# Performance work log

Measured on AMD Instinct MI355X. Metric: run time of the kernel, lower is better.

## Reference

```python
import jax, jax.numpy as jnp
import numpy as np

D = 128
NG = 100_000   # gene nodes
ND = 20_000    # disease nodes
EGG = 1_000_000  # gene->gene edges
EGD = 500_000    # gene->disease edges
NEG_SLOPE = 0.2  # PyG GATv2Conv default


def setup_inputs() -> dict:
    key = jax.random.key(0)
    ks = jax.random.split(key, 16)
    f = lambda k, shape, s=1.0: jax.random.normal(k, shape, dtype=jnp.float32) * s
    return {
        "x_gene": f(ks[0], (NG, D)),
        "x_dis": f(ks[1], (ND, D)),
        "src_gg": jax.random.randint(ks[2], (EGG,), 0, NG, dtype=jnp.int32),
        "dst_gg": jax.random.randint(ks[3], (EGG,), 0, NG, dtype=jnp.int32),
        "src_gd": jax.random.randint(ks[4], (EGD,), 0, NG, dtype=jnp.int32),
        "dst_gd": jax.random.randint(ks[5], (EGD,), 0, ND, dtype=jnp.int32),
        # stacked over the 2 layers: [layer, ...]
        "Wsrc_gg": f(ks[6], (2, D, D), 0.1),
        "Wdst_gg": f(ks[7], (2, D, D), 0.1),
        "att_gg": f(ks[8], (2, D), 0.1),
        "b_gg": f(ks[9], (2, D), 0.1),
        "Wsrc_gd": f(ks[10], (2, D, D), 0.1),
        "Wdst_gd": f(ks[11], (2, D, D), 0.1),
        "att_gd": f(ks[12], (2, D), 0.1),
        "b_gd": f(ks[13], (2, D), 0.1),
    }


def _gatv2(x_src, x_dst, src, dst, Wsrc, Wdst, att, b, n_dst):
    """PyG GATv2Conv, heads=1, add_self_loops=False."""
    xl = x_src @ Wsrc            # [Ns, D] source transform (lin_l)
    xr = x_dst @ Wdst            # [Nd, D] target transform (lin_r)
    e = jax.nn.leaky_relu(xl[src] + xr[dst], NEG_SLOPE)   # [E, D]
    score = e @ att                                        # [E]
    # segment softmax over incoming edges of each destination node
    m = jax.ops.segment_max(score, dst, num_segments=n_dst)
    a = jnp.exp(score - m[dst])
    s = jax.ops.segment_sum(a, dst, num_segments=n_dst)
    alpha = a / s[dst]                                     # [E]
    out = jax.ops.segment_sum(alpha[:, None] * xl[src], dst, num_segments=n_dst)
    return out + b


def reference(x_gene, x_dis, src_gg, dst_gg, src_gd, dst_gd,
              Wsrc_gg, Wdst_gg, att_gg, b_gg,
              Wsrc_gd, Wdst_gd, att_gd, b_gd):
    xg, xd = x_gene, x_dis
    for l in range(2):  # num_gat_layers=2, structurally distinct weights
        ng = _gatv2(xg, xg, src_gg, dst_gg, Wsrc_gg[l], Wdst_gg[l],
                    att_gg[l], b_gg[l], xg.shape[0])
        nd = _gatv2(xg, xd, src_gd, dst_gd, Wsrc_gd[l], Wdst_gd[l],
                    att_gd[l], b_gd[l], xd.shape[0])
        xg, xd = ng, nd  # HeteroConv: each node type receives from one edge type; aggr='sum' trivially
    # concatenate node-type outputs so the result is a single array
    return jnp.concatenate([xg, xd], axis=0)
```

## Files before the change

### kernel.cpp

```cpp
#include <hip/hip_runtime.h>

#define NGn 100000
#define NDn 20000
#define EGGn 1000000
#define EGDn 500000
#define Dn 128
#define NT (NGn + NDn)
#define ET (EGGn + EGDn)
#define NBK ((NT + 255) / 256)
#define P2B 128
#define CHUNK ((ET + P2B - 1) / P2B)

typedef unsigned short u16;
typedef unsigned int u32;
typedef __attribute__((ext_vector_type(8))) short short8;
typedef __attribute__((ext_vector_type(4))) float f32x4;

__device__ __forceinline__ float blo(u32 u) { return __uint_as_float(u << 16); }
__device__ __forceinline__ float bhi(u32 u) { return __uint_as_float(u & 0xffff0000u); }
__device__ __forceinline__ u16 f2bf(float f) {
    u32 u = __float_as_uint(f);
    u32 r = (u + 0x7fffu + ((u >> 16) & 1u)) >> 16;
    return (u16)r;
}

__device__ __forceinline__ int probe_bf16(const u16* __restrict__ x) {
    int lane = threadIdx.x & 63;
    u16 v = x[2 * lane];
    int e = (v >> 7) & 0xFF;
    unsigned long long m = __ballot(e >= 110 && e <= 135);
    return __popcll(m) >= 32;
}

#define NBX 15000
#define NBW 12
__global__ __launch_bounds__(256) void prep_all(
    const void* __restrict__ xg0, const void* __restrict__ xd0,
    const void* w0, const void* w1, const void* w2, const void* w3,
    const void* a0, const void* a1, const void* a2, const void* a3,
    u16* __restrict__ og, u16* __restrict__ od,
    u16* __restrict__ wbT, u16* __restrict__ vb,
    const int* __restrict__ dst_gg, const int* __restrict__ dst_gd,
    u32* __restrict__ bucketCnt)
{
    __shared__ u32 hist[NBK];
    int bx = blockIdx.x;
    int t = threadIdx.x;
    if (bx < NBX) {
        int f = probe_bf16((const u16*)xg0);
        if (f) return;
        int i4 = (bx * 256 + t) * 4;
        const int n1 = NGn * Dn;
        const float4* src; u16* dst; int j4;
        if (i4 < n1) { src = (const float4*)xg0; dst = og; j4 = i4; }
        else         { src = (const float4*)xd0; dst = od; j4 = i4 - n1; }
        float4 v = src[j4 >> 2];
        uint2 pack;
        pack.x = (u32)f2bf(v.x) | ((u32)f2bf(v.y) << 16);
        pack.y = (u32)f2bf(v.z) | ((u32)f2bf(v.w) << 16);
        *reinterpret_cast<uint2*>(dst + j4) = pack;
    } else if (bx < NBX + NBW) {
        int f = probe_bf16((const u16*)xg0);
        int sub = bx - NBX;
        if (sub < 8) {
            const void* srcs[4] = {w0, w1, w2, w3};
            const void* sp = srcs[sub >> 1];
            int ebase = (sub & 1) * (Dn * Dn);
            size_t mbase = (size_t)sub * (Dn * Dn);
            for (int i = t; i < Dn * Dn; i += 256) {
                u16 v = f ? ((const u16*)sp)[ebase + i] : f2bf(((const float*)sp)[ebase + i]);
                wbT[mbase + (size_t)((i & 127) << 7) + (i >> 7)] = v;
            }
        } else {
            const void* srcs[4] = {a0, a1, a2, a3};
            const void* sp = srcs[sub - 8];
            u16 v = f ? ((const u16*)sp)[t] : f2bf(((const float*)sp)[t]);
            vb[(sub - 8) * 256 + t] = v;
        }
    } else {
        int sub = bx - NBX - NBW;
        for (int i = t; i < NBK; i += 256) hist[i] = 0;
        __syncthreads();
        int lo = sub * CHUNK, hi = min(ET, lo + CHUNK);
        for (int i = lo + t; i < hi; i += 256) {
            int d = (i < EGGn) ? dst_gg[i] : (NGn + dst_gd[i - EGGn]);
            atomicAdd(&hist[d >> 8], 1u);
        }
        __syncthreads();
        for (int i = t; i < NBK; i += 256)
            if (hist[i]) atomicAdd(&bucketCnt[i], hist[i]);
    }
}

__global__ __launch_bounds__(256) void scan_buckets(
    const u32* __restrict__ bucketCnt, u32* __restrict__ bbase, u32* __restrict__ bcur)
{
    __shared__ u32 sh[256];
    int t = threadIdx.x;
    u32 carry = 0;
    for (int base = 0; base < NBK; base += 256) {
        int i = base + t;
        u32 v = (i < NBK) ? bucketCnt[i] : 0;
        sh[t] = v;
        __syncthreads();
#pragma unroll
        for (int off = 1; off < 256; off <<= 1) {
            u32 a = (t >= off) ? sh[t - off] : 0;
            __syncthreads();
            sh[t] += a;
            __syncthreads();
        }
        if (i < NBK) { u32 e = carry + sh[t] - v; bbase[i] = e; bcur[i] = e; }
        u32 chunk = sh[255];
        __syncthreads();
        carry += chunk;
    }
    if (t == 0) bbase[NBK] = carry;
}

#define GG_BLK ((NGn + 63) / 64)
#define GD_BLK ((NDn + 63) / 64)
#define LDB(KS) do { \
    b0 = Wof[0*256 + (KS)*4]; b1 = Wof[1*256 + (KS)*4]; \
    b2 = Wof[2*256 + (KS)*4]; b3 = Wof[3*256 + (KS)*4]; \
    b4 = Wof[4*256 + (KS)*4]; b5 = Wof[5*256 + (KS)*4]; \
    b6 = Wof[6*256 + (KS)*4]; b7 = Wof[7*256 + (KS)*4]; } while (0)
#define MFMA8(A) do { \
    c0 = __builtin_amdgcn_mfma_f32_16x16x32_bf16(A, b0, c0, 0, 0, 0); \
    c1 = __builtin_amdgcn_mfma_f32_16x16x32_bf16(A, b1, c1, 0, 0, 0); \
    c2 = __builtin_amdgcn_mfma_f32_16x16x32_bf16(A, b2, c2, 0, 0, 0); \
    c3 = __builtin_amdgcn_mfma_f32_16x16x32_bf16(A, b3, c3, 0, 0, 0); \
    c4 = __builtin_amdgcn_mfma_f32_16x16x32_bf16(A, b4, c4, 0, 0, 0); \
    c5 = __builtin_amdgcn_mfma_f32_16x16x32_bf16(A, b5, c5, 0, 0, 0); \
    c6 = __builtin_amdgcn_mfma_f32_16x16x32_bf16(A, b6, c6, 0, 0, 0); \
    c7 = __builtin_amdgcn_mfma_f32_16x16x32_bf16(A, b7, c7, 0, 0, 0); } while (0)
#define STORE_NT(NT, CV) do { \
    int cidx = (NT)*16 + r; \
    int rw0 = row0 + g*4; \
    if (rw0 + 0 < M) Y[(size_t)(rw0 + 0) * Dn + cidx] = f2bf(CV[0]); \
    if (rw0 + 1 < M) Y[(size_t)(rw0 + 1) * Dn + cidx] = f2bf(CV[1]); \
    if (rw0 + 2 < M) Y[(size_t)(rw0 + 2) * Dn + cidx] = f2bf(CV[2]); \
    if (rw0 + 3 < M) Y[(size_t)(rw0 + 3) * Dn + cidx] = f2bf(CV[3]); } while (0)

__device__ __forceinline__ void gemm_body(
    int gbx,
    const u16* __restrict__ Xg, const u16* __restrict__ Xd,
    const u16* __restrict__ WTg0, const u16* __restrict__ WTg1, const u16* __restrict__ WTg2,
    const u16* __restrict__ WTd,
    u16* __restrict__ Y0, u16* __restrict__ Y1, u16* __restrict__ Y2, u16* __restrict__ Y3)
{
    int wv = threadIdx.x >> 6, lane = threadIdx.x & 63;
    int r = lane & 15, g = lane >> 4;
    bool gene = gbx < GG_BLK;
    int blk = gene ? gbx : gbx - GG_BLK;
    int M = gene ? NGn : NDn;
    const u16* X = gene ? Xg : Xd;
    int row0 = blk * 64 + wv * 16;
    if (row0 >= M) return;
    int arow = row0 + r; if (arow >= M) arow = M - 1;
    const short8* Xa = reinterpret_cast<const short8*>(X + (size_t)arow * Dn);
    short8 a0 = Xa[g], a1 = Xa[4 + g], a2 = Xa[8 + g], a3 = Xa[12 + g];

    int no = gene ? 3 : 1;
    for (int o = 0; o < no; ++o) {
        const u16* Wt = gene ? ((o == 0) ? WTg0 : (o == 1) ? WTg1 : WTg2) : WTd;
        u16* Y = gene ? ((o == 0) ? Y0 : (o == 1) ? Y1 : Y2) : Y3;
        const short8* Wof = reinterpret_cast<const short8*>(Wt) + (size_t)r * 16 + g;
        f32x4 c0 = {0,0,0,0}, c1 = {0,0,0,0}, c2 = {0,0,0,0}, c3 = {0,0,0,0};
        f32x4 c4 = {0,0,0,0}, c5 = {0,0,0,0}, c6 = {0,0,0,0}, c7 = {0,0,0,0};
        short8 b0, b1, b2, b3, b4, b5, b6, b7;
        LDB(0); MFMA8(a0);
        LDB(1); MFMA8(a1);
        LDB(2); MFMA8(a2);
        LDB(3); MFMA8(a3);
        STORE_NT(0, c0); STORE_NT(1, c1); STORE_NT(2, c2); STORE_NT(3, c3);
        STORE_NT(4, c4); STORE_NT(5, c5); STORE_NT(6, c6); STORE_NT(7, c7);
    }
}

__global__ __launch_bounds__(256) void scatter_gemm(
    const int* __restrict__ src_gg, const int* __restrict__ dst_gg,
    const int* __restrict__ src_gd, const int* __restrict__ dst_gd,
    u32* __restrict__ bcur, u32* __restrict__ staging,
    const u16* __restrict__ xg0, const u16* __restrict__ xd0,
    const u16* __restrict__ Xgc, const u16* __restrict__ Xdc,
    const u16* __restrict__ WTg0, const u16* __restrict__ WTg1, const u16* __restrict__ WTg2,
    const u16* __restrict__ WTd,
    u16* __restrict__ Y0, u16* __restrict__ Y1, u16* __restrict__ Y2, u16* __restrict__ Y3)
{
    __shared__ u32 hist[NBK];
    __shared__ u32 lbase[NBK];
    int bx = blockIdx.x;
    if (bx < P2B) {
        int t = threadIdx.x;
        for (int i = t; i < NBK; i += 256) hist[i] = 0;
        __syncthreads();
        int lo = bx * CHUNK, hi = min(ET, lo + CHUNK);
        for (int i = lo + t; i < hi; i += 256) {
            int d = (i < EGGn) ? dst_gg[i] : (NGn + dst_gd[i - EGGn]);
            atomicAdd(&hist[d >> 8], 1u);
        }
        __syncthreads();
        for (int i = t; i < NBK; i += 256)
            lbase[i] = hist[i] ? atomicAdd(&bcur[i], hist[i]) : 0;
        __syncthreads();
        for (int i = t; i < NBK; i += 256) hist[i] = 0;
        __syncthreads();
        for (int i = lo + t; i < hi; i += 256) {
            int s, d;
            if (i < EGGn) { s = src_gg[i]; d = dst_gg[i]; }
            else          { s = src_gd[i - EGGn]; d = NGn + dst_gd[i - EGGn]; }
            int bk = d >> 8;
            u32 off = atomicAdd(&hist[bk], 1u);
            staging[lbase[bk] + off] = ((u32)s << 8) | (u32)(d & 255);
        }
    } else {
        int f = probe_bf16(xg0);
        const u16* Xg = f ? xg0 : Xgc;
        const u16* Xd = f ? xd0 : Xdc;
        gemm_body(bx - P2B, Xg, Xd, WTg0, WTg1, WTg2, WTd, Y0, Y1, Y2, Y3);
    }
}

__global__ __launch_bounds__(256) void fine_csr(
    const u32* __restrict__ bbase, const u32* __restrict__ staging,
    u32* __restrict__ rp, u32* __restrict__ deg, int* __restrict__ col)
{
    __shared__ u32 hist[256];
    __shared__ u32 sh[256];
    __shared__ u32 ex[256];
    int b = blockIdx.x, t = threadIdx.x;
    int base = (int)bbase[b], end = (int)bbase[b + 1];
    hist[t] = 0;
    __syncthreads();
    for (int i = base + t; i < end; i += 256)
        atomicAdd(&hist[staging[i] & 255u], 1u);
    __syncthreads();
    u32 v = hist[t];
    sh[t] = v;
    __syncthreads();
#pragma unroll
    for (int off = 1; off < 256; off <<= 1) {
        u32 a = (t >= off) ? sh[t - off] : 0;
        __syncthreads();
        sh[t] += a;
        __syncthreads();
    }
    ex[t] = sh[t] - v;
    int node = b * 256 + t;
    if (node < NT) { deg[node] = v; rp[node] = base + ex[t]; }
    hist[t] = 0;
    __syncthreads();
    for (int i = base + t; i < end; i += 256) {
        u32 pv = staging[i];
        u32 n = pv & 255u;
        u32 off2 = atomicAdd(&hist[n], 1u);
        col[base + ex[n] + off2] = (int)(pv >> 8);
    }
}

__global__ __launch_bounds__(256) void gemm_only(
    const u16* __restrict__ Xg, const u16* __restrict__ Xd,
    const u16* __restrict__ WTg0, const u16* __restrict__ WTg1, const u16* __restrict__ WTg2,
    const u16* __restrict__ WTd,
    u16* __restrict__ Y0, u16* __restrict__ Y1, u16* __restrict__ Y2, u16* __restrict__ Y3)
{
    gemm_body(blockIdx.x, Xg, Xd, WTg0, WTg1, WTg2, WTd, Y0, Y1, Y2, Y3);
}

#define SCORE8(RV, VALID, SC) do {                                                   \
    float x0_=blo(RV.x), x1_=bhi(RV.x), x2_=blo(RV.y), x3_=bhi(RV.y);                \
    float x4_=blo(RV.z), x5_=bhi(RV.z), x6_=blo(RV.w), x7_=bhi(RV.w);                \
    float t0_ = x0_ + xr0; t0_ = fmaxf(t0_, 0.2f * t0_);                             \
    float t1_ = x1_ + xr1; t1_ = fmaxf(t1_, 0.2f * t1_);                             \
    float t2_ = x2_ + xr2; t2_ = fmaxf(t2_, 0.2f * t2_);                             \
    float t3_ = x3_ + xr3; t3_ = fmaxf(t3_, 0.2f * t3_);                             \
    float t4_ = x4_ + xr4; t4_ = fmaxf(t4_, 0.2f * t4_);                             \
    float t5_ = x5_ + xr5; t5_ = fmaxf(t5_, 0.2f * t5_);                             \
    float t6_ = x6_ + xr6; t6_ = fmaxf(t6_, 0.2f * t6_);                             \
    float t7_ = x7_ + xr7; t7_ = fmaxf(t7_, 0.2f * t7_);                             \
    float sc_ = t0_*at0 + t1_*at1 + t2_*at2 + t3_*at3                                \
              + t4_*at4 + t5_*at5 + t6_*at6 + t7_*at7;                               \
    sc_ += __shfl_xor(sc_, 4);                                                       \
    sc_ += __shfl_xor(sc_, 8);                                                       \
    sc_ += __shfl_xor(sc_, 16);                                                      \
    sc_ += __shfl_xor(sc_, 32);                                                      \
    SC = (VALID) ? sc_ : -1.0e30f;                                                   \
} while (0)

__global__ __launch_bounds__(256) void gat_gather(
    const u16* __restrict__ xl_g, const u16* __restrict__ xr_g,
    const u16* __restrict__ xl_d, const u16* __restrict__ xr_d,
    const u32* __restrict__ rp, const u32* __restrict__ deg, const int* __restrict__ col,
    const u16* __restrict__ vb, int l,
    void* __restrict__ yg, void* __restrict__ yd,
    const u16* __restrict__ xg0probe, int to_out)
{
    int wv = threadIdx.x >> 6, lane = threadIdx.x & 63;
    bool gg = blockIdx.x < 25000;
    int blk = gg ? blockIdx.x : blockIdx.x - 25000;
    int d = blk * 4 + wv;
    int N = gg ? NGn : NDn;
    if (d >= N) return;
    const u16* xl_sel = gg ? xl_g : xl_d;
    const u16* xr_sel = gg ? xr_g : xr_d;
    int nodeid = d + (gg ? 0 : NGn);
    const u16* att = vb + (gg ? 0 : 512) + l * Dn;
    const u16* bv  = vb + (gg ? 256 : 768) + l * Dn;
    void* y = gg ? yg : yd;
    size_t yoff = (gg || !to_out) ? 0 : (size_t)NGn * Dn;

    int h = lane & 3;
    int qq = lane >> 2;

    uint4 rv = *reinterpret_cast<const uint4*>(xr_sel + (size_t)d * Dn + qq * 8);
    float xr0 = blo(rv.x), xr1 = bhi(rv.x), xr2 = blo(rv.y), xr3 = bhi(rv.y);
    float xr4 = blo(rv.z), xr5 = bhi(rv.z), xr6 = blo(rv.w), xr7 = bhi(rv.w);
    const float L2E = 1.44269504f;
    uint4 av = *reinterpret_cast<const uint4*>(att + qq * 8);
    float at0 = blo(av.x) * L2E, at1 = bhi(av.x) * L2E;
    float at2 = blo(av.y) * L2E, at3 = bhi(av.y) * L2E;
    float at4 = blo(av.z) * L2E, at5 = bhi(av.z) * L2E;
    float at6 = blo(av.w) * L2E, at7 = bhi(av.w) * L2E;

    int p0 = (int)rp[nodeid], p1 = p0 + (int)deg[nodeid];
    float s = 0.f;
    float ac0 = 0.f, ac1 = 0.f, ac2 = 0.f, ac3 = 0.f;
    float ac4 = 0.f, ac5 = 0.f, ac6 = 0.f, ac7 = 0.f;

    uint4 ra = make_uint4(0,0,0,0), rb = make_uint4(0,0,0,0);
    bool va = false, vb2 = false;
    if (p0 < p1) {
        int ea = p0 + h;     va  = ea < p1;
        int eb = p0 + h + 4; vb2 = eb < p1;
        int sa = col[va  ? ea : p0];
        int sb = col[vb2 ? eb : p0];
        ra = *reinterpret_cast<const uint4*>(xl_sel + (size_t)sa * Dn + qq * 8);
        rb = *reinterpret_cast<const uint4*>(xl_sel + (size_t)sb * Dn + qq * 8);
    }
    for (int pb = p0; pb < p1; pb += 8) {
        uint4 na = make_uint4(0,0,0,0), nb = make_uint4(0,0,0,0);
        bool vna = false, vnb = false;
        if (pb + 8 < p1) {
            int ea = pb + 8 + h;     vna = ea < p1;
            int eb = pb + 8 + h + 4; vnb = eb < p1;
            int sa = col[vna ? ea : p0];
            int sb = col[vnb ? eb : p0];
            na = *reinterpret_cast<const uint4*>(xl_sel + (size_t)sa * Dn + qq * 8);
            nb = *reinterpret_cast<const uint4*>(xl_sel + (size_t)sb * Dn + qq * 8);
        }
        float sca, scb;
        SCORE8(ra, va, sca);
        SCORE8(rb, vb2, scb);
        float pea = __builtin_amdgcn_exp2f(sca);
        float peb = __builtin_amdgcn_exp2f(scb);
        s += pea + peb;
        ac0 += pea * blo(ra.x) + peb * blo(rb.x);
        ac1 += pea * bhi(ra.x) + peb * bhi(rb.x);
        ac2 += pea * blo(ra.y) + peb * blo(rb.y);
        ac3 += pea * bhi(ra.y) + peb * bhi(rb.y);
        ac4 += pea * blo(ra.z) + peb * blo(rb.z);
        ac5 += pea * bhi(ra.z) + peb * bhi(rb.z);
        ac6 += pea * blo(ra.w) + peb * blo(rb.w);
        ac7 += pea * bhi(ra.w) + peb * bhi(rb.w);
        ra = na; rb = nb; va = vna; vb2 = vnb;
    }
    s   += __shfl_xor(s, 1);   s   += __shfl_xor(s, 2);
    ac0 += __shfl_xor(ac0, 1); ac0 += __shfl_xor(ac0, 2);
    ac1 += __shfl_xor(ac1, 1); ac1 += __shfl_xor(ac1, 2);
    ac2 += __shfl_xor(ac2, 1); ac2 += __shfl_xor(ac2, 2);
    ac3 += __shfl_xor(ac3, 1); ac3 += __shfl_xor(ac3, 2);
    ac4 += __shfl_xor(ac4, 1); ac4 += __shfl_xor(ac4, 2);
    ac5 += __shfl_xor(ac5, 1); ac5 += __shfl_xor(ac5, 2);
    ac6 += __shfl_xor(ac6, 1); ac6 += __shfl_xor(ac6, 2);
    ac7 += __shfl_xor(ac7, 1); ac7 += __shfl_xor(ac7, 2);
    float inv = (s > 0.f) ? __builtin_amdgcn_rcpf(s) : 0.f;
    uint4 bu = *reinterpret_cast<const uint4*>(bv + qq * 8);
    float o0 = ac0 * inv + blo(bu.x), o1 = ac1 * inv + bhi(bu.x);
    float o2 = ac2 * inv + blo(bu.y), o3 = ac3 * inv + bhi(bu.y);
    float o4 = ac4 * inv + blo(bu.z), o5 = ac5 * inv + bhi(bu.z);
    float o6 = ac6 * inv + blo(bu.w), o7 = ac7 * inv + bhi(bu.w);
    if (h != 0) return;
    int f = to_out ? probe_bf16(xg0probe) : 1;
    if (to_out && f == 0) {
        float* yf = (float*)y + yoff + (size_t)d * Dn + qq * 8;
        *reinterpret_cast<float4*>(yf)     = make_float4(o0, o1, o2, o3);
        *reinterpret_cast<float4*>(yf + 4) = make_float4(o4, o5, o6, o7);
    } else {
        uint4 pack;
        pack.x = (u32)f2bf(o0) | ((u32)f2bf(o1) << 16);
        pack.y = (u32)f2bf(o2) | ((u32)f2bf(o3) << 16);
        pack.z = (u32)f2bf(o4) | ((u32)f2bf(o5) << 16);
        pack.w = (u32)f2bf(o6) | ((u32)f2bf(o7) << 16);
        *reinterpret_cast<uint4*>((u16*)y + yoff + (size_t)d * Dn + qq * 8) = pack;
    }
}

extern "C" void kernel_launch(void* const* d_in, const int* in_sizes, int n_in,
                              void* d_out, int out_size, void* d_ws, size_t ws_size,
                              hipStream_t stream) {
    (void)in_sizes; (void)n_in; (void)out_size;
    const void* xg0     = d_in[0];
    const void* xd0     = d_in[1];
    const int* src_gg   = (const int*)d_in[2];
    const int* dst_gg   = (const int*)d_in[3];
    const int* src_gd   = (const int*)d_in[4];
    const int* dst_gd   = (const int*)d_in[5];
    const void* Wsrc_gg = d_in[6];
    const void* Wdst_gg = d_in[7];
    const void* att_gg  = d_in[8];
    const void* b_gg    = d_in[9];
    const void* Wsrc_gd = d_in[10];
    const void* Wdst_gd = d_in[11];
    const void* att_gd  = d_in[12];
    const void* b_gd    = d_in[13];

    char* base = (char*)d_ws;
    size_t off = 0;
    auto alloc = [&](size_t bytes) -> void* {
        void* r = base + off;
        off += (bytes + 255) & ~(size_t)255;
        return r;
    };
    u16*   wbT     = (u16*)  alloc((size_t)8 * Dn * Dn * 2);
    u16*   vb      = (u16*)  alloc((size_t)4 * 256 * 2);
    u16*   xg_bf   = (u16*)  alloc((size_t)NGn * Dn * 2);
    u16*   xd_bf   = (u16*)  alloc((size_t)NDn * Dn * 2);
    u16*   xl_gg   = (u16*)  alloc((size_t)NGn * Dn * 2);
    u16*   xr_gg   = (u16*)  alloc((size_t)NGn * Dn * 2);
    u16*   xl_gd   = (u16*)  alloc((size_t)NGn * Dn * 2);
    u16*   xr_gd   = (u16*)  alloc((size_t)NDn * Dn * 2);
    u32*   bucketCnt = (u32*)alloc((size_t)NBK * 4);
    u32*   bbase   = (u32*)  alloc((size_t)(NBK + 1) * 4);
    u32*   bcur    = (u32*)  alloc((size_t)NBK * 4);
    u32*   staging = (u32*)  alloc((size_t)ET * 4);
    u32*   rp      = (u32*)  alloc((size_t)NT * 4);
    u32*   deg     = (u32*)  alloc((size_t)NT * 4);
    int*   col     = (int*)  alloc((size_t)ET * 4);
    if (off > ws_size) return;

    hipMemsetAsync(bucketCnt, 0, (size_t)NBK * 4, stream);
    prep_all<<<NBX + NBW + P2B, 256, 0, stream>>>(
        xg0, xd0, Wsrc_gg, Wdst_gg, Wsrc_gd, Wdst_gd,
        att_gg, b_gg, att_gd, b_gd,
        xg_bf, xd_bf, wbT, vb, dst_gg, dst_gd, bucketCnt);
    scan_buckets<<<1, 256, 0, stream>>>(bucketCnt, bbase, bcur);

    const u16* wT = wbT;
    scatter_gemm<<<P2B + GG_BLK + GD_BLK, 256, 0, stream>>>(
        src_gg, dst_gg, src_gd, dst_gd, bcur, staging,
        (const u16*)xg0, (const u16*)xd0, xg_bf, xd_bf,
        wT + (size_t)(0 * 2 + 0) * Dn * Dn, wT + (size_t)(1 * 2 + 0) * Dn * Dn,
        wT + (size_t)(2 * 2 + 0) * Dn * Dn, wT + (size_t)(3 * 2 + 0) * Dn * Dn,
        xl_gg, xr_gg, xl_gd, xr_gd);
    fine_csr<<<NBK, 256, 0, stream>>>(bbase, staging, rp, deg, col);

    gat_gather<<<30000, 256, 0, stream>>>(
        xl_gg, xr_gg, xl_gd, xr_gd, rp, deg, col, vb, 0,
        xg_bf, xd_bf, (const u16*)xg0, 0);

    gemm_only<<<GG_BLK + GD_BLK, 256, 0, stream>>>(
        xg_bf, xd_bf,
        wT + (size_t)(0 * 2 + 1) * Dn * Dn, wT + (size_t)(1 * 2 + 1) * Dn * Dn,
        wT + (size_t)(2 * 2 + 1) * Dn * Dn, wT + (size_t)(3 * 2 + 1) * Dn * Dn,
        xl_gg, xr_gg, xl_gd, xr_gd);
    gat_gather<<<30000, 256, 0, stream>>>(
        xl_gg, xr_gg, xl_gd, xr_gd, rp, deg, col, vb, 1,
        d_out, d_out, (const u16*)xg0, 1);
}
```

Measured before the change: 462.3 us.

## Precompute per-block bucket offsets via count matrix and raise partition blocks

The prep kernel now stores each partition block's bucket histogram in a count matrix, and a new sub_scan kernel computes exclusive per-block base offsets for every bucket. The scatter kernel reads these offsets directly instead of rebuilding the histogram and doing global atomics on bucket cursors, so one pass over the dst arrays is removed. The number of partition blocks goes from 128 to 512 for more parallelism per chunk. The cost is an extra kernel launch, two P2B×NBK matrices of memory traffic, and sub_scan now assumes exactly 512 partition blocks (2 per thread).

```diff
diff --git a/kernel.cpp b/kernel.cpp
--- a/kernel.cpp
+++ b/kernel.cpp
@@ -8,7 +8,7 @@
 #define NT (NGn + NDn)
 #define ET (EGGn + EGDn)
 #define NBK ((NT + 255) / 256)
-#define P2B 128
+#define P2B 512
 #define CHUNK ((ET + P2B - 1) / P2B)
 
 typedef unsigned short u16;
@@ -41,7 +41,7 @@
     u16* __restrict__ og, u16* __restrict__ od,
     u16* __restrict__ wbT, u16* __restrict__ vb,
     const int* __restrict__ dst_gg, const int* __restrict__ dst_gd,
-    u32* __restrict__ bucketCnt)
+    u32* __restrict__ bucketCnt, u32* __restrict__ cntMat)
 {
     __shared__ u32 hist[NBK];
     int bx = blockIdx.x;
@@ -87,13 +87,16 @@
             atomicAdd(&hist[d >> 8], 1u);
         }
         __syncthreads();
-        for (int i = t; i < NBK; i += 256)
-            if (hist[i]) atomicAdd(&bucketCnt[i], hist[i]);
+        for (int i = t; i < NBK; i += 256) {
+            u32 h = hist[i];
+            cntMat[(size_t)sub * NBK + i] = h;
+            if (h) atomicAdd(&bucketCnt[i], h);
+        }
     }
 }
 
 __global__ __launch_bounds__(256) void scan_buckets(
-    const u32* __restrict__ bucketCnt, u32* __restrict__ bbase, u32* __restrict__ bcur)
+    const u32* __restrict__ bucketCnt, u32* __restrict__ bbase)
 {
     __shared__ u32 sh[256];
     int t = threadIdx.x;
@@ -110,12 +113,35 @@
             sh[t] += a;
             __syncthreads();
         }
-        if (i < NBK) { u32 e = carry + sh[t] - v; bbase[i] = e; bcur[i] = e; }
+        if (i < NBK) bbase[i] = carry + sh[t] - v;
         u32 chunk = sh[255];
         __syncthreads();
         carry += chunk;
     }
     if (t == 0) bbase[NBK] = carry;
+}
+
+__global__ __launch_bounds__(256) void sub_scan(
+    const u32* __restrict__ cntMat, const u32* __restrict__ bbase, u32* __restrict__ baseMat)
+{
+    __shared__ u32 sh[256];
+    int b = blockIdx.x, t = threadIdx.x;
+    u32 v0 = cntMat[(size_t)(2 * t) * NBK + b];
+    u32 v1 = cntMat[(size_t)(2 * t + 1) * NBK + b];
+    u32 pair = v0 + v1;
+    sh[t] = pair;
+    __syncthreads();
+#pragma unroll
+    for (int off = 1; off < 256; off <<= 1) {
+        u32 a = (t >= off) ? sh[t - off] : 0;
+        __syncthreads();
+        sh[t] += a;
+        __syncthreads();
+    }
+    u32 excl = sh[t] - pair;
+    u32 bb = bbase[b];
+    baseMat[(size_t)(2 * t) * NBK + b]     = bb + excl;
+    baseMat[(size_t)(2 * t + 1) * NBK + b] = bb + excl + v0;
 }
 
 #define GG_BLK ((NGn + 63) / 64)
@@ -181,37 +207,30 @@
 __global__ __launch_bounds__(256) void scatter_gemm(
     const int* __restrict__ src_gg, const int* __restrict__ dst_gg,
     const int* __restrict__ src_gd, const int* __restrict__ dst_gd,
-    u32* __restrict__ bcur, u32* __restrict__ staging,
+    const u32* __restrict__ baseMat, u32* __restrict__ staging,
     const u16* __restrict__ xg0, const u16* __restrict__ xd0,
     const u16* __restrict__ Xgc, const u16* __restrict__ Xdc,
     const u16* __restrict__ WTg0, const u16* __restrict__ WTg1, const u16* __restrict__ WTg2,
     const u16* __restrict__ WTd,
     u16* __restrict__ Y0, u16* __restrict__ Y1, u16* __restrict__ Y2, u16* __restrict__ Y3)
 {
-    __shared__ u32 hist[NBK];
+    __shared__ u32 cur[NBK];
     __shared__ u32 lbase[NBK];
     int bx = blockIdx.x;
     if (bx < P2B) {
         int t = threadIdx.x;
-        for (int i = t; i < NBK; i += 256) hist[i] = 0;
+        for (int i = t; i < NBK; i += 256) {
+            lbase[i] = baseMat[(size_t)bx * NBK + i];
+            cur[i] = 0;
+        }
         __syncthreads();
         int lo = bx * CHUNK, hi = min(ET, lo + CHUNK);
-        for (int i = lo + t; i < hi; i += 256) {
-            int d = (i < EGGn) ? dst_gg[i] : (NGn + dst_gd[i - EGGn]);
-            atomicAdd(&hist[d >> 8], 1u);
-        }
-        __syncthreads();
-        for (int i = t; i < NBK; i += 256)
-            lbase[i] = hist[i] ? atomicAdd(&bcur[i], hist[i]) : 0;
-        __syncthreads();
-        for (int i = t; i < NBK; i += 256) hist[i] = 0;
-        __syncthreads();
         for (int i = lo + t; i < hi; i += 256) {
             int s, d;
             if (i < EGGn) { s = src_gg[i]; d = dst_gg[i]; }
             else          { s = src_gd[i - EGGn]; d = NGn + dst_gd[i - EGGn]; }
             int bk = d >> 8;
-            u32 off = atomicAdd(&hist[bk], 1u);
+            u32 off = atomicAdd(&cur[bk], 1u);
             staging[lbase[bk] + off] = ((u32)s << 8) | (u32)(d & 255);
         }
     } else {
@@ -432,7 +451,8 @@
     u16*   xr_gd   = (u16*)  alloc((size_t)NDn * Dn * 2);
     u32*   bucketCnt = (u32*)alloc((size_t)NBK * 4);
     u32*   bbase   = (u32*)  alloc((size_t)(NBK + 1) * 4);
-    u32*   bcur    = (u32*)  alloc((size_t)NBK * 4);
+    u32*   cntMat  = (u32*)  alloc((size_t)P2B * NBK * 4);
+    u32*   baseMat = (u32*)  alloc((size_t)P2B * NBK * 4);
     u32*   staging = (u32*)  alloc((size_t)ET * 4);
     u32*   rp      = (u32*)  alloc((size_t)NT * 4);
     u32*   deg     = (u32*)  alloc((size_t)NT * 4);
@@ -443,12 +463,13 @@
     prep_all<<<NBX + NBW + P2B, 256, 0, stream>>>(
         xg0, xd0, Wsrc_gg, Wdst_gg, Wsrc_gd, Wdst_gd,
         att_gg, b_gg, att_gd, b_gd,
-        xg_bf, xd_bf, wbT, vb, dst_gg, dst_gd, bucketCnt);
-    scan_buckets<<<1, 256, 0, stream>>>(bucketCnt, bbase, bcur);
+        xg_bf, xd_bf, wbT, vb, dst_gg, dst_gd, bucketCnt, cntMat);
+    scan_buckets<<<1, 256, 0, stream>>>(bucketCnt, bbase);
+    sub_scan<<<NBK, 256, 0, stream>>>(cntMat, bbase, baseMat);
 
     const u16* wT = wbT;
     scatter_gemm<<<P2B + GG_BLK + GD_BLK, 256, 0, stream>>>(
-        src_gg, dst_gg, src_gd, dst_gd, bcur, staging,
+        src_gg, dst_gg, src_gd, dst_gd, baseMat, staging,
         (const u16*)xg0, (const u16*)xd0, xg_bf, xd_bf,
         wT + (size_t)(0 * 2 + 0) * Dn * Dn, wT + (size_t)(1 * 2 + 0) * Dn * Dn,
         wT + (size_t)(2 * 2 + 0) * Dn * Dn, wT + (size_t)(3 * 2 + 0) * Dn * Dn,
```

Result: slower. 483.1 us (+4.5%).
